# Kernel tuning notes

Hardware: AMD Instinct MI355X
Metric: run time of the kernel (lower is better)

Reference implementation:

```python
import jax, jax.numpy as jnp
import numpy as np

B, T, D, H, L, VOC = 2, 2048, 512, 8, 4, 32000
SLOTS = [16384, 8192, 4096]  # base_slots=16384, halved per level
KTOP = 4


def setup_inputs() -> dict:
    key = jax.random.key(0)
    ks = jax.random.split(key, 20)

    def n(i, shape, scale=0.02):
        return jax.random.normal(ks[i], shape, jnp.float32) * scale

    inp = {
        'input_ids': jax.random.randint(ks[0], (B, T), 0, VOC),
        'tok_embed': n(1, (VOC, D)),
        'pos_embed': n(2, (T, D)),
        'Wqkv': n(3, (L, 3 * D, D)), 'bqkv': jnp.zeros((L, 3 * D), jnp.float32),
        'Wo': n(4, (L, D, D)), 'bo': jnp.zeros((L, D), jnp.float32),
        'ln1_s': jnp.ones((L, D), jnp.float32), 'ln1_b': jnp.zeros((L, D), jnp.float32),
        'W1': n(5, (L, 4 * D, D)), 'b1': jnp.zeros((L, 4 * D), jnp.float32),
        'W2': n(6, (L, D, 4 * D)), 'b2': jnp.zeros((L, D), jnp.float32),
        'ln2_s': jnp.ones((L, D), jnp.float32), 'ln2_b': jnp.zeros((L, D), jnp.float32),
        'Wq': n(7, (D, D)), 'bq': jnp.zeros((D,), jnp.float32),
        'Wrp': n(8, (D, D)), 'brp': jnp.zeros((D,), jnp.float32),
        'lnout_s': jnp.ones((D,), jnp.float32), 'lnout_b': jnp.zeros((D,), jnp.float32),
    }
    # hierarchical memory banks (xavier-ish scale)
    for li, s in enumerate(SLOTS):
        inp[f'K{li}'] = n(10 + li, (s, D), float(1.0 / np.sqrt(D)))
        inp[f'V{li}'] = n(13 + li, (s, D), float(1.0 / np.sqrt(D)))
        inp[f's{li}'] = jnp.zeros((s,), jnp.float32)
    return inp


def _ln(x, s, b):
    m = x.mean(-1, keepdims=True)
    v = jnp.mean((x - m) ** 2, -1, keepdims=True)
    return (x - m) / jnp.sqrt(v + 1e-5) * s + b


def reference(input_ids, tok_embed, pos_embed, Wqkv, bqkv, Wo, bo, ln1_s, ln1_b,
              W1, b1, W2, b2, ln2_s, ln2_b, Wq, bq, Wrp, brp, lnout_s, lnout_b,
              K0, V0, s0, K1, V1, s1, K2, V2, s2):
    hd = D // H
    x = tok_embed[input_ids] + pos_embed[None, :, :]  # [B,T,D]
    for i in range(L):
        qkv = x @ Wqkv[i].T + bqkv[i]
        q, k, v = jnp.split(qkv, 3, -1)
        q = q.reshape(B, T, H, hd)
        k = k.reshape(B, T, H, hd)
        v = v.reshape(B, T, H, hd)
        att = jax.nn.softmax(jnp.einsum('bqhd,bkhd->bhqk', q, k) / np.float32(np.sqrt(hd)), -1)
        o = jnp.einsum('bhqk,bkhd->bqhd', att, v).reshape(B, T, D)
        x = _ln(x + (o @ Wo[i].T + bo[i]), ln1_s[i], ln1_b[i])
        f = jax.nn.gelu(x @ W1[i].T + b1[i], approximate=False) @ W2[i].T + b2[i]
        x = _ln(x + f, ln2_s[i], ln2_b[i])
    # hierarchical memory read (top-k gather attention per level)
    qm = x @ Wq.T + bq
    inv_sqrt_d = np.float32(1.0 / np.sqrt(D))
    read = jnp.zeros_like(x)
    for (K, V, sal) in ((K0, V0, s0), (K1, V1, s1), (K2, V2, s2)):
        scores = jnp.einsum('btd,sd->bts', qm, K) * inv_sqrt_d + sal  # [B,T,S]
        ts, ti = jax.lax.top_k(scores, KTOP)
        a = jax.nn.softmax(ts, -1)                 # [B,T,k]
        read = read + jnp.einsum('btk,btkd->btd', a, V[ti])  # gather + reduce
    read = read / np.float32(len(SLOTS))           # uniform level weights 1/num_levels
    x = x + (read @ Wrp.T + brp)
    x = _ln(x, lnout_s, lnout_b)
    return x @ tok_embed.T                          # tied lm_head [B,T,VOC]
```

## Files before the change

kernel.cpp:

```cpp
#include <hip/hip_runtime.h>
#include <cstdint>

typedef __bf16 bf16_t;
typedef __bf16 bf16x2 __attribute__((ext_vector_type(2)));
typedef __bf16 bf16x4 __attribute__((ext_vector_type(4)));
typedef __bf16 bf16x8 __attribute__((ext_vector_type(8)));
typedef float f32x4 __attribute__((ext_vector_type(4)));
typedef unsigned short u16;
typedef unsigned int u32;
typedef unsigned short u16x8 __attribute__((ext_vector_type(8)));

#define DEVI static __device__ __forceinline__

DEVI void g2l16(const void* g, void* l) {
  __builtin_amdgcn_global_load_lds((__attribute__((address_space(1))) void*)g,
                                   (__attribute__((address_space(3))) void*)l,
                                   16, 0, 0);
}

DEVI void tki4(u32* k, u32 nk) {
  if (nk <= k[3]) return;
  k[3] = nk;
  if (k[3] > k[2]) { u32 t = k[2]; k[2] = k[3]; k[3] = t; }
  if (k[2] > k[1]) { u32 t = k[1]; k[1] = k[2]; k[2] = t; }
  if (k[1] > k[0]) { u32 t = k[0]; k[0] = k[1]; k[1] = t; }
}

struct F2BArgs {
  const float* s[10];
  bf16_t* d[10];
  int n4[10];
};
__global__ void k_f2b_all(F2BArgs a) {
  const int seg = blockIdx.y;
  const float* __restrict__ in = a.s[seg];
  bf16_t* __restrict__ out = a.d[seg];
  const long n4 = a.n4[seg];
  const long stride = (long)gridDim.x * blockDim.x;
  for (long i = (long)blockIdx.x * blockDim.x + threadIdx.x; i < n4; i += stride) {
    float4 v = ((const float4*)in)[i];
    bf16x4 o = {(bf16_t)v.x, (bf16_t)v.y, (bf16_t)v.z, (bf16_t)v.w};
    ((bf16x4*)out)[i] = o;
  }
}

__global__ void k_embed(const int* __restrict__ ids, const float* __restrict__ tok,
                        const float* __restrict__ pos, float* __restrict__ x,
                        bf16_t* __restrict__ xb) {
  int r = blockIdx.x;
  int t = r & 2047;
  long id = ids[r];
  int d = threadIdx.x * 2;
  float2 a = *(const float2*)(tok + id * 512 + d);
  float2 p = *(const float2*)(pos + (long)t * 512 + d);
  float o0 = a.x + p.x, o1 = a.y + p.y;
  *(float2*)(x + (long)r * 512 + d) = make_float2(o0, o1);
  bf16x2 ob = {(bf16_t)o0, (bf16_t)o1};
  *(bf16x2*)(xb + (long)r * 512 + d) = ob;
}

DEVI float gelu_f(float f) {
  return 0.5f * f * (1.0f + erff(f * 0.70710678118654752f));
}

template <typename CT, bool BIAS, int EPI>
__global__ __launch_bounds__(256, 2) void k_gemm_bt(
    const bf16_t* __restrict__ A, int lda, const bf16_t* __restrict__ B, int ldb,
    CT* __restrict__ C, int ldc, const float* __restrict__ bias, int K, float alpha,
    bf16_t* __restrict__ qh, bf16_t* __restrict__ kh, bf16_t* __restrict__ vt) {
  __shared__ bf16_t As[4096];
  __shared__ bf16_t Bs[4096];
  const int tid = threadIdx.x;
  const int lane = tid & 63;
  const int w = tid >> 6;
  const int wm = w >> 1, wn = w & 1;
  const int m0 = blockIdx.y * 128;
  const int n0 = blockIdx.x * 128;

  f32x4 acc[4][4];
#pragma unroll
  for (int m = 0; m < 4; ++m)
#pragma unroll
    for (int n = 0; n < 4; ++n) acc[m][n] = (f32x4){0.f, 0.f, 0.f, 0.f};

  const int srow = tid >> 2;
  const int scol = ((tid & 3) ^ ((srow >> 1) & 3)) * 8;
  const int fr = lane & 15;
  const int g4 = lane >> 4;
  const int kg = g4 * 8;

  for (int k0 = 0; k0 < K; k0 += 32) {
#pragma unroll
    for (int p = 0; p < 2; ++p) {
      g2l16(A + (long long)(m0 + p * 64 + srow) * lda + (k0 + scol), As + p * 2048 + w * 512);
      g2l16(B + (long long)(n0 + p * 64 + srow) * ldb + (k0 + scol), Bs + p * 2048 + w * 512);
    }
    __syncthreads();
    bf16x8 fa[4], fb[4];
#pragma unroll
    for (int m = 0; m < 4; ++m) {
      const int row = wm * 64 + m * 16 + fr;
      fa[m] = *(const bf16x8*)(As + row * 32 + (kg ^ (((row >> 1) & 3) << 3)));
    }
#pragma unroll
    for (int n = 0; n < 4; ++n) {
      const int row = wn * 64 + n * 16 + fr;
      fb[n] = *(const bf16x8*)(Bs + row * 32 + (kg ^ (((row >> 1) & 3) << 3)));
    }
#pragma unroll
    for (int m = 0; m < 4; ++m)
#pragma unroll
      for (int n = 0; n < 4; ++n)
        acc[m][n] = __builtin_amdgcn_mfma_f32_16x16x32_bf16(fa[m], fb[n], acc[m][n], 0, 0, 0);
    __syncthreads();
  }

#pragma unroll
  for (int n = 0; n < 4; ++n) {
    const int col = n0 + wn * 64 + n * 16 + fr;
    const float bv = BIAS ? bias[col] : 0.0f;
    if (EPI == 1) {
      const int reg = col >> 9;
      const int h = (col >> 6) & 7;
      const int hd = col & 63;
#pragma unroll
      for (int m = 0; m < 4; ++m) {
        const int rb = m0 + wm * 64 + m * 16 + g4 * 4;
#pragma unroll
        for (int r = 0; r < 4; ++r) {
          const int row = rb + r;
          const int b = row >> 11, t = row & 2047;
          const long long bh = (long long)b * 8 + h;
          float v = acc[m][n][r] + bv;
          if (reg == 0) qh[(bh * 2048 + t) * 64 + hd] = (bf16_t)(v * 0.125f);
          else if (reg == 1) kh[(bh * 2048 + t) * 64 + hd] = (bf16_t)v;
          else vt[(bh * 64 + hd) * 2048 + t] = (bf16_t)v;
        }
      }
    } else {
#pragma unroll
      for (int m = 0; m < 4; ++m) {
        const long long rb = m0 + wm * 64 + m * 16 + g4 * 4;
#pragma unroll
        for (int r = 0; r < 4; ++r) {
          float v = (acc[m][n][r] + bv) * alpha;
          if (EPI == 2) v = gelu_f(v);
          C[(rb + r) * (long long)ldc + col] = (CT)v;
        }
      }
    }
  }
}

template <typename CT, bool BIAS>
__global__ __launch_bounds__(256, 4) void k_gemm64(
    const bf16_t* __restrict__ A, int lda, const bf16_t* __restrict__ B, int ldb,
    CT* __restrict__ C, int ldc, long long sCz, const float* __restrict__ bias,
    int K, float alpha) {
  __shared__ bf16_t As[64 * 32];
  __shared__ bf16_t Bs[128 * 32];
  const int tid = threadIdx.x;
  const int lane = tid & 63;
  const int w = tid >> 6;
  const int wm = w >> 1, wn = w & 1;
  const int m0 = blockIdx.y * 64;
  const int n0 = blockIdx.x * 128;
  const int kz = blockIdx.z;
  A += (long long)kz * K;
  B += (long long)kz * K;
  C += (long long)kz * sCz;

  f32x4 acc[2][4];
#pragma unroll
  for (int m = 0; m < 2; ++m)
#pragma unroll
    for (int n = 0; n < 4; ++n) acc[m][n] = (f32x4){0.f, 0.f, 0.f, 0.f};

  const int srow = tid >> 2;
  const int scol = ((tid & 3) ^ ((srow >> 1) & 3)) * 8;
  const int fr = lane & 15;
  const int g4 = lane >> 4;
  const int kg = g4 * 8;

  for (int k0 = 0; k0 < K; k0 += 32) {
    g2l16(A + (long long)(m0 + srow) * lda + (k0 + scol), As + tid * 8);
    g2l16(B + (long long)(n0 + srow) * ldb + (k0 + scol), Bs + tid * 8);
    g2l16(B + (long long)(n0 + 64 + srow) * ldb + (k0 + scol), Bs + 2048 + tid * 8);
    __syncthreads();
    bf16x8 fa[2], fb[4];
#pragma unroll
    for (int m = 0; m < 2; ++m) {
      const int row = wm * 32 + m * 16 + fr;
      fa[m] = *(const bf16x8*)(As + row * 32 + (kg ^ (((row >> 1) & 3) << 3)));
    }
#pragma unroll
    for (int n = 0; n < 4; ++n) {
      const int row = wn * 64 + n * 16 + fr;
      fb[n] = *(const bf16x8*)(Bs + row * 32 + (kg ^ (((row >> 1) & 3) << 3)));
    }
#pragma unroll
    for (int m = 0; m < 2; ++m)
#pragma unroll
      for (int n = 0; n < 4; ++n)
        acc[m][n] = __builtin_amdgcn_mfma_f32_16x16x32_bf16(fa[m], fb[n], acc[m][n], 0, 0, 0);
    __syncthreads();
  }

#pragma unroll
  for (int n = 0; n < 4; ++n) {
    const int col = n0 + wn * 64 + n * 16 + fr;
    const float bv = (BIAS && kz == 0) ? bias[col] : 0.0f;
#pragma unroll
    for (int m = 0; m < 2; ++m) {
      const long long rb = m0 + wm * 32 + m * 16 + g4 * 4;
#pragma unroll
      for (int r = 0; r < 4; ++r)
        C[(rb + r) * (long long)ldc + col] = (CT)((acc[m][n][r] + bv) * alpha);
    }
  }
}

template <typename CT, int EPI>
__global__ __launch_bounds__(512, 2) void k_gemm256(
    const bf16_t* __restrict__ A, int lda, const bf16_t* __restrict__ B, int ldb,
    CT* __restrict__ C, int ldc, int K, float alpha,
    const float* __restrict__ s0, const float* __restrict__ s1,
    const float* __restrict__ s2, u32* __restrict__ cand) {
  __shared__ char lds[131072];
  const int tid = threadIdx.x;
  const int lane = tid & 63;
  const int w = tid >> 6;
  const int wm = w >> 2, wn = w & 3;
  const int fr = lane & 15;
  const int g4 = lane >> 4;

  const int ny = gridDim.y;
  const int nwg = gridDim.x * ny;
  int orig = blockIdx.y * gridDim.x + blockIdx.x;
  int lin = ((nwg & 7) == 0) ? ((orig & 7) * (nwg >> 3) + (orig >> 3)) : orig;
  const int m0 = (lin % ny) * 256;
  const int n0 = (lin / ny) * 256;

  f32x4 acc[8][4];
#pragma unroll
  for (int m = 0; m < 8; ++m)
#pragma unroll
    for (int n = 0; n < 4; ++n) acc[m][n] = (f32x4){0.f, 0.f, 0.f, 0.f};

  const int sr = tid >> 2;
  const int sc = (tid & 3) * 16;
  const int NT = K >> 6;

  auto stage = [&](int t, int p, int buf) {
    const long long kb = (long long)t * 128 + p * 64;
    char* ab = (char*)lds + buf * 65536 + p * 16384;
    char* bb = ab + 32768;
    const int sw = ((sr >> 1) & 3) << 4;
    g2l16((const char*)A + (long long)(m0 + sr) * (lda * 2) + kb + (sc ^ sw), ab + tid * 16);
    g2l16((const char*)A + (long long)(m0 + 128 + sr) * (lda * 2) + kb + (sc ^ sw),
          ab + (tid + 512) * 16);
    g2l16((const char*)B + (long long)(n0 + sr) * (ldb * 2) + kb + (sc ^ sw), bb + tid * 16);
    g2l16((const char*)B + (long long)(n0 + 128 + sr) * (ldb * 2) + kb + (sc ^ sw),
          bb + (tid + 512) * 16);
  };

  stage(0, 0, 0);
  stage(0, 1, 0);
  asm volatile("s_waitcnt vmcnt(4)" ::: "memory");
  __builtin_amdgcn_s_barrier();
  __builtin_amdgcn_sched_barrier(0);

  int cur = 0;
  for (int t = 0; t < NT; ++t) {
#pragma unroll
    for (int p = 0; p < 2; ++p) {
      const char* ab = (const char*)lds + cur * 65536 + p * 16384;
      const char* bb = ab + 32768;
      bf16x8 fa[8], fb[4];
#pragma unroll
      for (int m = 0; m < 8; ++m) {
        const int row = wm * 128 + m * 16 + fr;
        fa[m] = *(const bf16x8*)(ab + row * 64 + ((g4 * 16) ^ (((row >> 1) & 3) << 4)));
      }
#pragma unroll
      for (int n = 0; n < 4; ++n) {
        const int row = wn * 64 + n * 16 + fr;
        fb[n] = *(const bf16x8*)(bb + row * 64 + ((g4 * 16) ^ (((row >> 1) & 3) << 4)));
      }
      if (t + 1 < NT) stage(t + 1, p, cur ^ 1);
      if (t == NT - 1 && p == 0) {
        asm volatile("s_waitcnt vmcnt(0)" ::: "memory");
      } else {
        asm volatile("s_waitcnt vmcnt(4)" ::: "memory");
      }
      __builtin_amdgcn_s_barrier();
      __builtin_amdgcn_sched_barrier(0);
      __builtin_amdgcn_s_setprio(1);
#pragma unroll
      for (int m = 0; m < 8; ++m)
#pragma unroll
        for (int n = 0; n < 4; ++n)
          acc[m][n] = __builtin_amdgcn_mfma_f32_16x16x32_bf16(fa[m], fb[n], acc[m][n], 0, 0, 0);
      __builtin_amdgcn_s_setprio(0);
    }
    cur ^= 1;
  }

  if (EPI == 0) {
#pragma unroll
    for (int n = 0; n < 4; ++n) {
      const int col = n0 + wn * 64 + n * 16 + fr;
#pragma unroll
      for (int m = 0; m < 8; ++m) {
        const long long rb = m0 + wm * 128 + m * 16 + g4 * 4;
#pragma unroll
        for (int r = 0; r < 4; ++r)
          C[(rb + r) * (long long)ldc + col] = (CT)(acc[m][n][r] * alpha);
      }
    }
  } else {
    const float* salp;
    if (n0 < 16384) salp = s0 + n0;
    else if (n0 < 24576) salp = s1 + (n0 - 16384);
    else salp = s2 + (n0 - 24576);
    float bv[4];
    int coll[4];
#pragma unroll
    for (int n = 0; n < 4; ++n) {
      coll[n] = wn * 64 + n * 16 + fr;
      bv[n] = salp[coll[n]];
    }
    __syncthreads();
    u16* slab = (u16*)lds;
#pragma unroll
    for (int m = 0; m < 8; ++m) {
#pragma unroll
      for (int r = 0; r < 4; ++r) {
        const int rl = wm * 128 + m * 16 + g4 * 4 + r;
        const int sw = (rl & 7) << 3;
#pragma unroll
        for (int n = 0; n < 4; ++n) {
          bf16_t bvv = (bf16_t)(acc[m][n][r] + bv[n]);
          slab[rl * 256 + (coll[n] ^ sw)] = __builtin_bit_cast(u16, bvv);
        }
      }
    }
    __syncthreads();
    const int rr = tid & 255;
    const int hh = tid >> 8;
    const int sw = (rr & 7) << 3;
    u32 rk[4] = {0u, 0u, 0u, 0u};
    const u32 ibase = 0x7FFFu - (u32)n0;
#pragma unroll
    for (int j = 0; j < 16; ++j) {
      const int c0 = hh * 128 + j * 8;
      u16x8 vv = *(const u16x8*)(slab + rr * 256 + (c0 ^ sw));
#pragma unroll
      for (int e = 0; e < 8; ++e) {
        u16 sb = vv[e];
        u32 k16 = (u32)sb ^ (0x8000u | (0x7FFFu * (u32)(sb >> 15)));
        tki4(rk, (k16 << 15) | (ibase - (u32)(c0 + e)));
      }
    }
    __syncthreads();
    u32* res = (u32*)lds;
#pragma unroll
    for (int j = 0; j < 4; ++j) res[(rr * 2 + hh) * 4 + j] = rk[j];
    __syncthreads();
    if (tid < 256) {
      const u32* rp = res + tid * 8;
      u32 fin[4] = {rp[0], rp[1], rp[2], rp[3]};
      tki4(fin, rp[4]); tki4(fin, rp[5]); tki4(fin, rp[6]); tki4(fin, rp[7]);
      u32* cp = cand + ((long long)(m0 + tid) * 112 + (n0 >> 8)) * 4;
#pragma unroll
      for (int j = 0; j < 4; ++j) cp[j] = fin[j];
    }
  }
}

__global__ __launch_bounds__(256, 3) void k_flash(
    const bf16_t* __restrict__ qh, const bf16_t* __restrict__ kh,
    const bf16_t* __restrict__ vt, bf16_t* __restrict__ out) {
  __shared__ bf16_t Ks[128 * 64];
  __shared__ bf16_t Vs[64 * 128];
  __shared__ bf16_t Ps[4 * 16 * 128];
  const int tid = threadIdx.x;
  const int lane = tid & 63;
  const int w = tid >> 6;
  const int bh = blockIdx.y;
  const int q0 = blockIdx.x * 64;
  const int fr = lane & 15;
  const int g4 = lane >> 4;
  const int kg = g4 * 8;

  bf16x8 qf[2];
  {
    const bf16_t* qb = qh + ((long long)bh * 2048 + q0 + w * 16) * 64;
#pragma unroll
    for (int ks = 0; ks < 2; ++ks)
      qf[ks] = *(const bf16x8*)(qb + fr * 64 + ks * 32 + kg);
  }

  f32x4 oacc[4];
#pragma unroll
  for (int n = 0; n < 4; ++n) oacc[n] = (f32x4){0.f, 0.f, 0.f, 0.f};
  float li[4] = {0.f, 0.f, 0.f, 0.f};

  char* PsW = (char*)(Ps + w * 16 * 128);
  const bf16_t* kbase = kh + (long long)bh * 2048 * 64;
  const bf16_t* vbase = vt + (long long)bh * 64 * 2048;

  for (int kt = 0; kt < 16; ++kt) {
#pragma unroll
    for (int i = 0; i < 4; ++i) {
      int row = (w * 4 + i) * 8 + (lane >> 3);
      int c = lane & 7;
      g2l16(kbase + ((long long)(kt * 128 + row)) * 64 + (c ^ (row & 7)) * 8,
            Ks + (w * 4 + i) * 512);
    }
#pragma unroll
    for (int i = 0; i < 4; ++i) {
      int d = w * 16 + i * 4 + (lane >> 4);
      int c = lane & 15;
      g2l16(vbase + (long long)d * 2048 + kt * 128 + ((c ^ (d & 7)) * 8),
            Vs + (w * 16 + i * 4) * 128);
    }
    __syncthreads();

    f32x4 s[8];
#pragma unroll
    for (int n = 0; n < 8; ++n) s[n] = (f32x4){0.f, 0.f, 0.f, 0.f};
#pragma unroll
    for (int ks = 0; ks < 2; ++ks) {
#pragma unroll
      for (int n = 0; n < 8; ++n) {
        int row = n * 16 + fr;
        bf16x8 kf = *(const bf16x8*)((const char*)Ks + row * 128 +
                                     ((ks * 64 + kg * 2) ^ ((row & 7) << 4)));
        s[n] = __builtin_amdgcn_mfma_f32_16x16x32_bf16(qf[ks], kf, s[n], 0, 0, 0);
      }
    }

#pragma unroll
    for (int r = 0; r < 4; ++r) {
      const int lr = g4 * 4 + r;
      const int sw = (lr & 7) << 4;
      float rs = 0.f;
#pragma unroll
      for (int n = 0; n < 8; ++n) {
        float p = __expf(s[n][r]);
        rs += p;
        *(bf16_t*)(PsW + lr * 256 + (((n * 16 + fr) * 2) ^ sw)) = (bf16_t)p;
      }
      li[r] += rs;
    }

#pragma unroll
    for (int ks = 0; ks < 4; ++ks) {
      bf16x8 pa = *(const bf16x8*)(PsW + fr * 256 +
                                   ((ks * 64 + kg * 2) ^ ((fr & 7) << 4)));
#pragma unroll
      for (int n = 0; n < 4; ++n) {
        int d = n * 16 + fr;
        bf16x8 vf = *(const bf16x8*)((const char*)Vs + d * 256 +
                                     ((ks * 64 + kg * 2) ^ ((d & 7) << 4)));
        oacc[n] = __builtin_amdgcn_mfma_f32_16x16x32_bf16(pa, vf, oacc[n], 0, 0, 0);
      }
    }
    __syncthreads();
  }

#pragma unroll
  for (int r = 0; r < 4; ++r) {
    li[r] += __shfl_xor(li[r], 1);
    li[r] += __shfl_xor(li[r], 2);
    li[r] += __shfl_xor(li[r], 4);
    li[r] += __shfl_xor(li[r], 8);
  }

  const int b = bh >> 3, h = bh & 7;
  bf16_t* ob = out + ((long long)b * 2048 + q0 + w * 16) * 512 + h * 64;
#pragma unroll
  for (int r = 0; r < 4; ++r) {
    float inv = 1.0f / li[r];
#pragma unroll
    for (int n = 0; n < 4; ++n)
      ob[(g4 * 4 + r) * 512 + n * 16 + fr] = (bf16_t)(oacc[n][r] * inv);
  }
}

__global__ void k_ln2(const float* __restrict__ xin, const float* __restrict__ d1,
                      const float* __restrict__ d2, const float* __restrict__ s,
                      const float* __restrict__ b, float* __restrict__ xout,
                      bf16_t* __restrict__ xbf) {
  __shared__ float red[8];
  const int r = blockIdx.x;
  const int tid = threadIdx.x;
  const int d = tid * 2;
  const int lane = tid & 63, w = tid >> 6;
  float2 xi = *(const float2*)(xin + (long)r * 512 + d);
  float2 e1 = *(const float2*)(d1 + (long)r * 512 + d);
  float2 e2 = *(const float2*)(d2 + (long)r * 512 + d);
  float y0 = xi.x + e1.x + e2.x, y1 = xi.y + e1.y + e2.y;
  float sum = y0 + y1, ss = y0 * y0 + y1 * y1;
#pragma unroll
  for (int o = 32; o > 0; o >>= 1) { sum += __shfl_xor(sum, o); ss += __shfl_xor(ss, o); }
  if (lane == 0) { red[w] = sum; red[4 + w] = ss; }
  __syncthreads();
  sum = red[0] + red[1] + red[2] + red[3];
  ss = red[4] + red[5] + red[6] + red[7];
  const float mean = sum * (1.0f / 512.0f);
  const float var = ss * (1.0f / 512.0f) - mean * mean;
  const float rstd = rsqrtf(var + 1e-5f);
  float o0 = (y0 - mean) * rstd * s[d] + b[d];
  float o1 = (y1 - mean) * rstd * s[d + 1] + b[d + 1];
  *(float2*)(xout + (long)r * 512 + d) = make_float2(o0, o1);
  bf16x2 ob = {(bf16_t)o0, (bf16_t)o1};
  *(bf16x2*)(xbf + (long)r * 512 + d) = ob;
}

__global__ void k_topk3(const u32* __restrict__ cand, float* __restrict__ tv,
                        int* __restrict__ ti) {
  const int r = blockIdx.x * 4 + (threadIdx.x >> 6);
  const int lane = threadIdx.x & 63;
  const u32* cr = cand + (long long)r * 448;
  int base = 0;
  for (int lev = 0; lev < 3; ++lev) {
    const int cnt = lev == 0 ? 256 : (lev == 1 ? 128 : 64);
    const int coff = lev == 0 ? 0 : (lev == 1 ? 16384 : 24576);
    u32 rk[4] = {0u, 0u, 0u, 0u};
    for (int j = lane; j < cnt; j += 64) tki4(rk, cr[base + j]);
    base += cnt;
#pragma unroll
    for (int dd = 1; dd < 64; dd <<= 1) {
      u32 o[4];
#pragma unroll
      for (int j = 0; j < 4; ++j) o[j] = (u32)__shfl_xor((int)rk[j], dd);
#pragma unroll
      for (int j = 0; j < 4; ++j) tki4(rk, o[j]);
    }
    if (lane == 0) {
      const long o = ((long)lev * 4096 + r) * 4;
#pragma unroll
      for (int j = 0; j < 4; ++j) {
        u32 k16 = rk[j] >> 15;
        u16 b = (k16 & 0x8000u) ? (u16)(k16 ^ 0x8000u) : (u16)(~k16);
        u32 fb = ((u32)b) << 16;
        tv[o + j] = __uint_as_float(fb);
        ti[o + j] = (0x7FFF - (int)(rk[j] & 0x7FFF)) - coff;
      }
    }
  }
}

__global__ void k_read(const float* __restrict__ tv, const int* __restrict__ ti,
                       const float* __restrict__ V0, const float* __restrict__ V1,
                       const float* __restrict__ V2, bf16_t* __restrict__ readb) {
  const int r = blockIdx.x;
  const int d = threadIdx.x * 2;
  float a0 = 0.f, a1 = 0.f;
  const float* Vs[3] = {V0, V1, V2};
  const int smax[3] = {16383, 8191, 4095};
#pragma unroll
  for (int lev = 0; lev < 3; ++lev) {
    const float* tvr = tv + ((long)lev * 4096 + r) * 4;
    const int* tir = ti + ((long)lev * 4096 + r) * 4;
    float t0 = tvr[0], t1 = tvr[1], t2 = tvr[2], t3 = tvr[3];
    float m = fmaxf(fmaxf(t0, t1), fmaxf(t2, t3));
    float e0 = __expf(t0 - m), e1 = __expf(t1 - m), e2 = __expf(t2 - m), e3 = __expf(t3 - m);
    float inv = 1.0f / (e0 + e1 + e2 + e3);
    float w4[4] = {e0 * inv, e1 * inv, e2 * inv, e3 * inv};
#pragma unroll
    for (int k = 0; k < 4; ++k) {
      int idx = tir[k];
      idx = idx < 0 ? 0 : (idx > smax[lev] ? smax[lev] : idx);
      const float* vr = Vs[lev] + (long)idx * 512;
      a0 += w4[k] * vr[d];
      a1 += w4[k] * vr[d + 1];
    }
  }
  bf16x2 o = {(bf16_t)(a0 * (1.0f / 3.0f)), (bf16_t)(a1 * (1.0f / 3.0f))};
  *(bf16x2*)(readb + (long)r * 512 + d) = o;
}

extern "C" void kernel_launch(void* const* d_in, const int* in_sizes, int n_in,
                              void* d_out, int out_size, void* d_ws, size_t ws_size,
                              hipStream_t stream) {
  (void)in_sizes; (void)n_in; (void)out_size; (void)ws_size;
  const int* ids = (const int*)d_in[0];
  const float* tok = (const float*)d_in[1];
  const float* pos = (const float*)d_in[2];
  const float* Wqkv = (const float*)d_in[3];
  const float* bqkv = (const float*)d_in[4];
  const float* Wo = (const float*)d_in[5];
  const float* bo = (const float*)d_in[6];
  const float* ln1s = (const float*)d_in[7];
  const float* ln1b = (const float*)d_in[8];
  const float* W1 = (const float*)d_in[9];
  const float* b1 = (const float*)d_in[10];
  const float* W2 = (const float*)d_in[11];
  const float* b2 = (const float*)d_in[12];
  const float* ln2s = (const float*)d_in[13];
  const float* ln2b = (const float*)d_in[14];
  const float* Wq = (const float*)d_in[15];
  const float* bq = (const float*)d_in[16];
  const float* Wrp = (const float*)d_in[17];
  const float* brp = (const float*)d_in[18];
  const float* lnos = (const float*)d_in[19];
  const float* lnob = (const float*)d_in[20];
  const float* K0 = (const float*)d_in[21];
  const float* V0 = (const float*)d_in[22];
  const float* s0 = (const float*)d_in[23];
  const float* K1 = (const float*)d_in[24];
  const float* V1 = (const float*)d_in[25];
  const float* s1 = (const float*)d_in[26];
  const float* K2 = (const float*)d_in[27];
  const float* V2 = (const float*)d_in[28];
  const float* s2 = (const float*)d_in[29];

  char* wp = (char*)d_ws;
  auto walloc = [&](size_t bytes) -> char* {
    char* p = wp; wp += (bytes + 255) & ~(size_t)255; return p;
  };
  char* op = (char*)d_out;
  auto oalloc = [&](size_t bytes) -> char* {
    char* p = op; op += (bytes + 255) & ~(size_t)255; return p;
  };

  bf16_t* Wqkvb = (bf16_t*)oalloc(3145728ULL * 2);
  bf16_t* Wob   = (bf16_t*)oalloc(1048576ULL * 2);
  bf16_t* W1b   = (bf16_t*)oalloc(4194304ULL * 2);
  bf16_t* W2b   = (bf16_t*)oalloc(4194304ULL * 2);
  bf16_t* Wqb   = (bf16_t*)oalloc(262144ULL * 2);
  bf16_t* Wrpb  = (bf16_t*)oalloc(262144ULL * 2);
  bf16_t* Kb    = (bf16_t*)oalloc(28672ULL * 512 * 2);
  bf16_t* hb    = (bf16_t*)oalloc(4096ULL * 2048 * 2);
  u32*    cand  = (u32*)oalloc(4096ULL * 112 * 4 * 4);
  float*  delta = (float*)oalloc(2ULL * 4096 * 512 * 4);

  bf16_t* tokb = (bf16_t*)walloc(16384000ULL * 2);
  float*  x    = (float*)walloc(4096ULL * 512 * 4);
  bf16_t* xb   = (bf16_t*)walloc(4096ULL * 512 * 2);
  bf16_t* qh   = (bf16_t*)walloc(2097152ULL * 2);
  bf16_t* kh   = (bf16_t*)walloc(2097152ULL * 2);
  bf16_t* vt   = (bf16_t*)walloc(2097152ULL * 2);
  bf16_t* attob = (bf16_t*)walloc(4096ULL * 512 * 2);
  bf16_t* qmb  = (bf16_t*)walloc(4096ULL * 512 * 2);
  bf16_t* readb = (bf16_t*)walloc(4096ULL * 512 * 2);
  float*  tval = (float*)walloc(3ULL * 4096 * 4 * 4);
  int*    tidx = (int*)walloc(3ULL * 4096 * 4 * 4);
  bf16_t* xfb  = (bf16_t*)walloc(4096ULL * 512 * 2);

  F2BArgs fa;
  fa.s[0] = tok;  fa.d[0] = tokb;  fa.n4[0] = 4096000;
  fa.s[1] = Wqkv; fa.d[1] = Wqkvb; fa.n4[1] = 786432;
  fa.s[2] = Wo;   fa.d[2] = Wob;   fa.n4[2] = 262144;
  fa.s[3] = W1;   fa.d[3] = W1b;   fa.n4[3] = 1048576;
  fa.s[4] = W2;   fa.d[4] = W2b;   fa.n4[4] = 1048576;
  fa.s[5] = Wq;   fa.d[5] = Wqb;   fa.n4[5] = 65536;
  fa.s[6] = Wrp;  fa.d[6] = Wrpb;  fa.n4[6] = 65536;
  fa.s[7] = K0;   fa.d[7] = Kb;                fa.n4[7] = 2097152;
  fa.s[8] = K1;   fa.d[8] = Kb + 8388608L;     fa.n4[8] = 1048576;
  fa.s[9] = K2;   fa.d[9] = Kb + 12582912L;    fa.n4[9] = 524288;
  k_f2b_all<<<dim3(128, 10), 256, 0, stream>>>(fa);

  k_embed<<<4096, 256, 0, stream>>>(ids, tok, pos, x, xb);

  const long long sCz = 4096LL * 512;
  for (int i = 0; i < 4; ++i) {
    k_gemm_bt<bf16_t, true, 1><<<dim3(12, 32), 256, 0, stream>>>(
        xb, 512, Wqkvb + (long long)i * 786432, 512, (bf16_t*)nullptr, 0,
        bqkv + i * 1536, 512, 1.0f, qh, kh, vt);
    k_flash<<<dim3(32, 16), 256, 0, stream>>>(qh, kh, vt, attob);
    k_gemm64<float, true><<<dim3(4, 64, 2), 256, 0, stream>>>(
        attob, 512, Wob + (long long)i * 262144, 512, delta, 512, sCz,
        bo + i * 512, 256, 1.0f);
    k_ln2<<<4096, 256, 0, stream>>>(x, delta, delta + sCz,
                                    ln1s + i * 512, ln1b + i * 512, x, xb);
    k_gemm_bt<bf16_t, true, 2><<<dim3(16, 32), 256, 0, stream>>>(
        xb, 512, W1b + (long long)i * 1048576, 512, hb, 2048,
        b1 + i * 2048, 512, 1.0f, nullptr, nullptr, nullptr);
    k_gemm64<float, true><<<dim3(4, 64, 2), 256, 0, stream>>>(
        hb, 2048, W2b + (long long)i * 1048576, 2048, delta, 512, sCz,
        b2 + i * 512, 1024, 1.0f);
    k_ln2<<<4096, 256, 0, stream>>>(x, delta, delta + sCz,
                                    ln2s + i * 512, ln2b + i * 512, x, xb);
  }

  k_gemm64<bf16_t, true><<<dim3(4, 64, 1), 256, 0, stream>>>(
      xb, 512, Wqb, 512, qmb, 512, 0LL, bq, 512, 0.044194173824159216f);
  k_gemm256<bf16_t, 1><<<dim3(112, 16), 512, 0, stream>>>(
      qmb, 512, Kb, 512, (bf16_t*)nullptr, 0, 512, 1.0f, s0, s1, s2, cand);
  k_topk3<<<1024, 256, 0, stream>>>(cand, tval, tidx);
  k_read<<<4096, 256, 0, stream>>>(tval, tidx, V0, V1, V2, readb);
  k_gemm64<float, true><<<dim3(4, 64, 2), 256, 0, stream>>>(
      readb, 512, Wrpb, 512, delta, 512, sCz, brp, 256, 1.0f);
  k_ln2<<<4096, 256, 0, stream>>>(x, delta, delta + sCz, lnos, lnob, x, xfb);
  k_gemm256<float, 0><<<dim3(125, 16), 512, 0, stream>>>(
      xfb, 512, tokb, 512, (float*)d_out, 32000, 512, 1.0f,
      nullptr, nullptr, nullptr, nullptr);
}
```

Measured before the change: 1.172 ms.

## Deepen 256-tile GEMM pipeline to 4-slot ring and double split-K

The 256x256 GEMM main loop moves from a double-buffered two-phase scheme to a 4-slot LDS ring with three K-chunks in flight, so global loads are issued further ahead of the MFMA work. Separately, the split-K GEMMs for the output projection, FFN down-projection and memory read projection now use 4 K-splits instead of 2. The layernorm kernel is generalized to sum four partial buffers, and it skips the fp32 write on the final call. More splits give more workgroups for these small-N GEMMs, at the cost of extra partial-sum traffic through the delta buffers.

```diff
diff --git a/kernel.cpp b/kernel.cpp
--- a/kernel.cpp
+++ b/kernel.cpp
@@ -249,12 +249,13 @@
 
   const int sr = tid >> 2;
   const int sc = (tid & 3) * 16;
-  const int NT = K >> 6;
-
-  auto stage = [&](int t, int p, int buf) {
-    const long long kb = (long long)t * 128 + p * 64;
-    char* ab = (char*)lds + buf * 65536 + p * 16384;
-    char* bb = ab + 32768;
+  const int NP = K >> 5;
+
+  auto stage = [&](int kp) {
+    const int slot = kp & 3;
+    const long long kb = (long long)kp * 64;
+    char* ab = (char*)lds + slot * 16384;
+    char* bb = (char*)lds + 65536 + slot * 16384;
     const int sw = ((sr >> 1) & 3) << 4;
     g2l16((const char*)A + (long long)(m0 + sr) * (lda * 2) + kb + (sc ^ sw), ab + tid * 16);
     g2l16((const char*)A + (long long)(m0 + 128 + sr) * (lda * 2) + kb + (sc ^ sw),
@@ -264,46 +265,45 @@
           bb + (tid + 512) * 16);
   };
 
-  stage(0, 0, 0);
-  stage(0, 1, 0);
-  asm volatile("s_waitcnt vmcnt(4)" ::: "memory");
+  stage(0);
+  stage(1);
+  stage(2);
+  asm volatile("s_waitcnt vmcnt(8)" ::: "memory");
   __builtin_amdgcn_s_barrier();
   __builtin_amdgcn_sched_barrier(0);
 
-  int cur = 0;
-  for (int t = 0; t < NT; ++t) {
-#pragma unroll
-    for (int p = 0; p < 2; ++p) {
-      const char* ab = (const char*)lds + cur * 65536 + p * 16384;
-      const char* bb = ab + 32768;
-      bf16x8 fa[8], fb[4];
-#pragma unroll
-      for (int m = 0; m < 8; ++m) {
-        const int row = wm * 128 + m * 16 + fr;
-        fa[m] = *(const bf16x8*)(ab + row * 64 + ((g4 * 16) ^ (((row >> 1) & 3) << 4)));
-      }
-#pragma unroll
-      for (int n = 0; n < 4; ++n) {
-        const int row = wn * 64 + n * 16 + fr;
-        fb[n] = *(const bf16x8*)(bb + row * 64 + ((g4 * 16) ^ (((row >> 1) & 3) << 4)));
-      }
-      if (t + 1 < NT) stage(t + 1, p, cur ^ 1);
-      if (t == NT - 1 && p == 0) {
-        asm volatile("s_waitcnt vmcnt(0)" ::: "memory");
-      } else {
-        asm volatile("s_waitcnt vmcnt(4)" ::: "memory");
-      }
-      __builtin_amdgcn_s_barrier();
-      __builtin_amdgcn_sched_barrier(0);
-      __builtin_amdgcn_s_setprio(1);
-#pragma unroll
-      for (int m = 0; m < 8; ++m)
-#pragma unroll
-        for (int n = 0; n < 4; ++n)
-          acc[m][n] = __builtin_amdgcn_mfma_f32_16x16x32_bf16(fa[m], fb[n], acc[m][n], 0, 0, 0);
-      __builtin_amdgcn_s_setprio(0);
-    }
-    cur ^= 1;
+  for (int k = 0; k < NP; ++k) {
+    const int slot = k & 3;
+    const char* ab = (const char*)lds + slot * 16384;
+    const char* bb = (const char*)lds + 65536 + slot * 16384;
+    bf16x8 fa[8], fb[4];
+#pragma unroll
+    for (int m = 0; m < 8; ++m) {
+      const int row = wm * 128 + m * 16 + fr;
+      fa[m] = *(const bf16x8*)(ab + row * 64 + ((g4 * 16) ^ (((row >> 1) & 3) << 4)));
+    }
+#pragma unroll
+    for (int n = 0; n < 4; ++n) {
+      const int row = wn * 64 + n * 16 + fr;
+      fb[n] = *(const bf16x8*)(bb + row * 64 + ((g4 * 16) ^ (((row >> 1) & 3) << 4)));
+    }
+    if (k + 3 < NP) stage(k + 3);
+    if (k <= NP - 4) {
+      asm volatile("s_waitcnt vmcnt(8)" ::: "memory");
+    } else if (k == NP - 3) {
+      asm volatile("s_waitcnt vmcnt(4)" ::: "memory");
+    } else {
+      asm volatile("s_waitcnt vmcnt(0)" ::: "memory");
+    }
+    __builtin_amdgcn_s_barrier();
+    __builtin_amdgcn_sched_barrier(0);
+    __builtin_amdgcn_s_setprio(1);
+#pragma unroll
+    for (int m = 0; m < 8; ++m)
+#pragma unroll
+      for (int n = 0; n < 4; ++n)
+        acc[m][n] = __builtin_amdgcn_mfma_f32_16x16x32_bf16(fa[m], fb[n], acc[m][n], 0, 0, 0);
+    __builtin_amdgcn_s_setprio(0);
   }
 
   if (EPI == 0) {
@@ -489,8 +489,8 @@
   }
 }
 
-__global__ void k_ln2(const float* __restrict__ xin, const float* __restrict__ d1,
-                      const float* __restrict__ d2, const float* __restrict__ s,
+__global__ void k_ln4(const float* __restrict__ xin, const float* __restrict__ dd,
+                      long long sCz, const float* __restrict__ s,
                       const float* __restrict__ b, float* __restrict__ xout,
                       bf16_t* __restrict__ xbf) {
   __shared__ float red[8];
@@ -499,9 +499,13 @@
   const int d = tid * 2;
   const int lane = tid & 63, w = tid >> 6;
   float2 xi = *(const float2*)(xin + (long)r * 512 + d);
-  float2 e1 = *(const float2*)(d1 + (long)r * 512 + d);
-  float2 e2 = *(const float2*)(d2 + (long)r * 512 + d);
-  float y0 = xi.x + e1.x + e2.x, y1 = xi.y + e1.y + e2.y;
+  float y0 = xi.x, y1 = xi.y;
+#pragma unroll
+  for (int z = 0; z < 4; ++z) {
+    float2 e = *(const float2*)(dd + z * sCz + (long)r * 512 + d);
+    y0 += e.x;
+    y1 += e.y;
+  }
   float sum = y0 + y1, ss = y0 * y0 + y1 * y1;
 #pragma unroll
   for (int o = 32; o > 0; o >>= 1) { sum += __shfl_xor(sum, o); ss += __shfl_xor(ss, o); }
@@ -514,7 +518,7 @@
   const float rstd = rsqrtf(var + 1e-5f);
   float o0 = (y0 - mean) * rstd * s[d] + b[d];
   float o1 = (y1 - mean) * rstd * s[d + 1] + b[d + 1];
-  *(float2*)(xout + (long)r * 512 + d) = make_float2(o0, o1);
+  if (xout) *(float2*)(xout + (long)r * 512 + d) = make_float2(o0, o1);
   bf16x2 ob = {(bf16_t)o0, (bf16_t)o1};
   *(bf16x2*)(xbf + (long)r * 512 + d) = ob;
 }
@@ -636,7 +640,7 @@
   bf16_t* Kb    = (bf16_t*)oalloc(28672ULL * 512 * 2);
   bf16_t* hb    = (bf16_t*)oalloc(4096ULL * 2048 * 2);
   u32*    cand  = (u32*)oalloc(4096ULL * 112 * 4 * 4);
-  float*  delta = (float*)oalloc(2ULL * 4096 * 512 * 4);
+  float*  delta = (float*)oalloc(4ULL * 4096 * 512 * 4);
 
   bf16_t* tokb = (bf16_t*)walloc(16384000ULL * 2);
   float*  x    = (float*)walloc(4096ULL * 512 * 4);
@@ -672,18 +676,18 @@
         xb, 512, Wqkvb + (long long)i * 786432, 512, (bf16_t*)nullptr, 0,
         bqkv + i * 1536, 512, 1.0f, qh, kh, vt);
     k_flash<<<dim3(32, 16), 256, 0, stream>>>(qh, kh, vt, attob);
-    k_gemm64<float, true><<<dim3(4, 64, 2), 256, 0, stream>>>(
+    k_gemm64<float, true><<<dim3(4, 64, 4), 256, 0, stream>>>(
         attob, 512, Wob + (long long)i * 262144, 512, delta, 512, sCz,
-        bo + i * 512, 256, 1.0f);
-    k_ln2<<<4096, 256, 0, stream>>>(x, delta, delta + sCz,
+        bo + i * 512, 128, 1.0f);
+    k_ln4<<<4096, 256, 0, stream>>>(x, delta, sCz,
                                     ln1s + i * 512, ln1b + i * 512, x, xb);
     k_gemm_bt<bf16_t, true, 2><<<dim3(16, 32), 256, 0, stream>>>(
         xb, 512, W1b + (long long)i * 1048576, 512, hb, 2048,
         b1 + i * 2048, 512, 1.0f, nullptr, nullptr, nullptr);
-    k_gemm64<float, true><<<dim3(4, 64, 2), 256, 0, stream>>>(
+    k_gemm64<float, true><<<dim3(4, 64, 4), 256, 0, stream>>>(
         hb, 2048, W2b + (long long)i * 1048576, 2048, delta, 512, sCz,
-        b2 + i * 512, 1024, 1.0f);
-    k_ln2<<<4096, 256, 0, stream>>>(x, delta, delta + sCz,
+        b2 + i * 512, 512, 1.0f);
+    k_ln4<<<4096, 256, 0, stream>>>(x, delta, sCz,
                                     ln2s + i * 512, ln2b + i * 512, x, xb);
   }
 
@@ -693,9 +697,9 @@
       qmb, 512, Kb, 512, (bf16_t*)nullptr, 0, 512, 1.0f, s0, s1, s2, cand);
   k_topk3<<<1024, 256, 0, stream>>>(cand, tval, tidx);
   k_read<<<4096, 256, 0, stream>>>(tval, tidx, V0, V1, V2, readb);
-  k_gemm64<float, true><<<dim3(4, 64, 2), 256, 0, stream>>>(
-      readb, 512, Wrpb, 512, delta, 512, sCz, brp, 256, 1.0f);
-  k_ln2<<<4096, 256, 0, stream>>>(x, delta, delta + sCz, lnos, lnob, x, xfb);
+  k_gemm64<float, true><<<dim3(4, 64, 4), 256, 0, stream>>>(
+      readb, 512, Wrpb, 512, delta, 512, sCz, brp, 128, 1.0f);
+  k_ln4<<<4096, 256, 0, stream>>>(x, delta, sCz, lnos, lnob, nullptr, xfb);
   k_gemm256<float, 0><<<dim3(125, 16), 512, 0, stream>>>(
       xfb, 512, tokb, 512, (float*)d_out, 32000, 512, 1.0f,
       nullptr, nullptr, nullptr, nullptr);
```

Measured after the change: 1.211 ms. +3.3%, slower.
